# Performance work log

Measured on AMD Instinct MI355X. Metric: run time of the kernel, lower is better.

## Reference

```python
import jax, jax.numpy as jnp
import numpy as np

# graph sizes: G graphs of N_PER nodes each (block-diagonal batched graph)
G, N_PER, F, NHID, E_PER = 128, 512, 128, 128, 4096
N = G * N_PER
E = G * E_PER
L1, L2, L3 = 4, 2, 2            # PANConv filter sizes (conv1 uses init filter_size=4)
K1, K2, K3 = N_PER // 2, N_PER // 4, N_PER // 8  # ratio=0.5 top-k per pooling stage


def setup_inputs() -> dict:
    ks = jax.random.split(jax.random.key(0), 10)
    rng = np.random.default_rng(0)
    off = (np.arange(G) * N_PER)[:, None]
    src = (rng.integers(0, N_PER, size=(G, E_PER)) + off).reshape(-1)
    dst = (rng.integers(0, N_PER, size=(G, E_PER)) + off).reshape(-1)
    edge_index = jnp.asarray(np.stack([src, dst]).astype(np.int32))
    batch = jnp.repeat(jnp.arange(G, dtype=jnp.int32), N_PER)
    def w(k, shp, fan):
        return jax.random.normal(k, shp, jnp.float32) / np.float32(np.sqrt(fan))
    z = lambda *s: jnp.zeros(s, jnp.float32)
    return dict(
        x=jax.random.normal(ks[0], (N, F), jnp.float32),
        edge_index=edge_index, batch=batch,
        lump_W=w(ks[1], (F, NHID), F), lump_b=z(NHID),
        conv1_W=w(ks[2], (NHID, NHID), NHID), conv1_b=z(NHID),
        conv2_W=w(ks[3], (NHID, NHID), NHID), conv2_b=z(NHID),
        conv3_W=w(ks[4], (NHID, NHID), NHID), conv3_b=z(NHID),
        pool1_p=w(ks[5], (NHID,), NHID), pool1_beta=jnp.full((2,), 0.5, jnp.float32),
        pool2_p=w(ks[6], (NHID,), NHID), pool2_beta=jnp.full((2,), 0.5, jnp.float32),
        pool3_p=w(ks[7], (NHID,), NHID), pool3_beta=jnp.full((2,), 0.5, jnp.float32),
        lin1_W=w(ks[8], (NHID, NHID // 2), NHID), lin1_b=z(NHID // 2),
        lin2_W=w(ks[9], (NHID // 2, 1), NHID // 2), lin2_b=z(1),
    )


def _pan_prop(h, src, dst, ew, L):
    # (sum_{l=0..L} A^l) @ h, A weighted by edge weights ew, via iterated gather/scatter
    acc, y = h, h
    n = h.shape[0]
    for _ in range(L):
        y = jax.ops.segment_sum(y[src] * ew[:, None], dst, num_segments=n)
        acc = acc + y
    return acc


def _pan_conv(x, src, dst, ew, W, b, L):
    # PANConv: M = Z^{-1/2} (sum_{l<=L} A^l) Z^{-1/2};  out = M x W + b
    d = _pan_prop(jnp.ones((x.shape[0], 1), x.dtype), src, dst, ew, L)[:, 0]
    dinv = jax.lax.rsqrt(jnp.maximum(d, 1e-12))
    h = dinv[:, None] * _pan_prop(dinv[:, None] * x, src, dst, ew, L)
    return h @ W + b


def _pan_pool(x, src, dst, ew, p, beta, n_per, k):
    # PANPooling: score = beta0*(x.p)/||p|| + beta1*node_strength; per-graph top-k
    n = x.shape[0]
    deg = jax.ops.segment_sum(ew, dst, num_segments=n)
    score = beta[0] * (x @ p) / jnp.linalg.norm(p) + beta[1] * deg
    _, idx = jax.lax.top_k(score.reshape(G, n_per), k)          # [G, k] local indices
    perm = (idx + (jnp.arange(G) * n_per)[:, None]).reshape(-1)  # [G*k] global
    x_new = x[perm] * jnp.tanh(score[perm])[:, None]
    inv = jnp.zeros((n,), jnp.int32).at[perm].set(jnp.arange(G * k, dtype=jnp.int32))
    mask = jnp.zeros((n,), x.dtype).at[perm].set(1.0)
    # keep edge arrays fixed-size: dropped edges get weight 0 (same math as filtering)
    return x_new, inv[src], inv[dst], ew * mask[src] * mask[dst], perm


def reference(x, edge_index, batch, lump_W, lump_b, conv1_W, conv1_b, conv2_W, conv2_b,
              conv3_W, conv3_b, pool1_p, pool1_beta, pool2_p, pool2_beta, pool3_p,
              pool3_beta, lin1_W, lin1_b, lin2_W, lin2_b):
    src, dst = edge_index[0], edge_index[1]
    ew = jnp.ones((src.shape[0],), x.dtype)
    h = x @ lump_W + lump_b                                   # PANLump lift
    h = _pan_conv(h, src, dst, ew, conv1_W, conv1_b, L1)
    h, src, dst, ew, perm1 = _pan_pool(h, src, dst, ew, pool1_p, pool1_beta, N_PER, K1)
    h = _pan_conv(h, src, dst, ew, conv2_W, conv2_b, L2)
    h, src, dst, ew, perm2 = _pan_pool(h, src, dst, ew, pool2_p, pool2_beta, K1, K2)
    h = _pan_conv(h, src, dst, ew, conv3_W, conv3_b, L3)
    h, src, dst, ew, perm3 = _pan_pool(h, src, dst, ew, pool3_p, pool3_beta, K2, K3)
    seg = jnp.repeat(jnp.arange(G, dtype=jnp.int32), K3)
    mean = jax.ops.segment_sum(h, seg, num_segments=G) / jnp.float32(K3)  # scatter_mean
    out = jax.nn.relu(mean @ lin1_W + lin1_b) @ lin2_W + lin2_b           # [G, 1]
    return out
```

## Files before the change

### kernel.cpp

```cpp
#include <hip/hip_runtime.h>
#include <math.h>

#define G_     128
#define E_     524288
#define EPG    4096
#define DEGMAX 48

typedef __attribute__((ext_vector_type(8))) short bf16x8;
typedef __attribute__((ext_vector_type(4))) float f32x4;
typedef __attribute__((ext_vector_type(4))) unsigned short u16x4;

__device__ inline void split_bf16(float x, short& hi, short& lo){
    unsigned u = __float_as_uint(x);
    hi = (short)(u >> 16);
    float hf = __uint_as_float(u & 0xffff0000u);
    unsigned r = __float_as_uint(x - hf);
    lo = (short)(r >> 16);
}

template<int WAVES>
__device__ void gemm_body(char* smem, int bid, const float* __restrict__ X,
        const float* __restrict__ W, const float* __restrict__ bias, float* __restrict__ Y,
        const float* __restrict__ p, const float* __restrict__ beta,
        const int* __restrict__ cntv, float* __restrict__ score){
    short* wsh = (short*)smem;
    short* wsl = (short*)(smem + 34816);
    float* bsh = (float*)(smem + 69632);
    float* qs  = (float*)(smem + 70144);
    float* rednorm = (float*)(smem + 70656);
    const int NT = WAVES*64;
    int t = threadIdx.x;
    for (int e = t; e < 16384; e += NT){
        int k = e >> 7, n = e & 127;
        short hi, lo; split_bf16(W[e], hi, lo);
        wsh[n*136 + k] = hi; wsl[n*136 + k] = lo;
    }
    if (t < 128) bsh[t] = bias[t];
    if (score && t < 64){ float a = p[t], b = p[t+64]; rednorm[t] = a*a + b*b; }
    __syncthreads();
    float b1 = 0.f;
    if (score){
        if (t == 0){ float s = 0.f; for (int i = 0; i < 64; i++) s += rednorm[i]; rednorm[0] = sqrtf(s); }
        __syncthreads();
        if (t < 128) qs[t] = beta[0] * p[t] / rednorm[0];
        b1 = beta[1];
        __syncthreads();
    }
    int wave = t >> 6, lane = t & 63;
    int ln = lane & 15, q = lane >> 4;
    size_t rb = (size_t)bid * (WAVES*16);
    const float* xrow = &X[(rb + wave*16 + ln)*128 + q*8];
    f32x4 acc[8];
    #pragma unroll
    for (int i = 0; i < 8; i++) acc[i] = (f32x4){0.f,0.f,0.f,0.f};
    #pragma unroll
    for (int kc = 0; kc < 4; kc++){
        float4 xa = *(const float4*)(xrow + kc*32);
        float4 xb = *(const float4*)(xrow + kc*32 + 4);
        bf16x8 ah, al; short hi, lo;
        split_bf16(xa.x, hi, lo); ah[0]=hi; al[0]=lo;
        split_bf16(xa.y, hi, lo); ah[1]=hi; al[1]=lo;
        split_bf16(xa.z, hi, lo); ah[2]=hi; al[2]=lo;
        split_bf16(xa.w, hi, lo); ah[3]=hi; al[3]=lo;
        split_bf16(xb.x, hi, lo); ah[4]=hi; al[4]=lo;
        split_bf16(xb.y, hi, lo); ah[5]=hi; al[5]=lo;
        split_bf16(xb.z, hi, lo); ah[6]=hi; al[6]=lo;
        split_bf16(xb.w, hi, lo); ah[7]=hi; al[7]=lo;
        #pragma unroll
        for (int nt = 0; nt < 8; nt++){
            int wo = (nt*16 + ln)*136 + kc*32 + q*8;
            bf16x8 bh = *(const bf16x8*)&wsh[wo];
            bf16x8 bl = *(const bf16x8*)&wsl[wo];
            acc[nt] = __builtin_amdgcn_mfma_f32_16x16x32_bf16(ah, bh, acc[nt], 0, 0, 0);
            acc[nt] = __builtin_amdgcn_mfma_f32_16x16x32_bf16(ah, bl, acc[nt], 0, 0, 0);
            acc[nt] = __builtin_amdgcn_mfma_f32_16x16x32_bf16(al, bh, acc[nt], 0, 0, 0);
        }
    }
    #pragma unroll
    for (int nt = 0; nt < 8; nt++){
        int c = nt*16 + ln;
        float bb = bsh[c];
        #pragma unroll
        for (int r = 0; r < 4; r++){
            Y[(rb + wave*16 + q*4 + r)*128 + c] = acc[nt][r] + bb;
        }
    }
    if (score){
        #pragma unroll
        for (int r = 0; r < 4; r++){
            float sp = 0.f;
            #pragma unroll
            for (int nt = 0; nt < 8; nt++){
                int c = nt*16 + ln;
                sp += (acc[nt][r] + bsh[c]) * qs[c];
            }
            sp += __shfl_xor(sp, 1);
            sp += __shfl_xor(sp, 2);
            sp += __shfl_xor(sp, 4);
            sp += __shfl_xor(sp, 8);
            if (ln == 0){
                int row = (int)rb + wave*16 + q*4 + r;
                score[row] = sp + b1 * (float)cntv[row];
            }
        }
    }
}

template<int WAVES>
__global__ __launch_bounds__(WAVES*64) void k_gemm_mfma(const float* __restrict__ X,
        const float* __restrict__ W, const float* __restrict__ bias, float* __restrict__ Y,
        const float* __restrict__ p, const float* __restrict__ beta,
        const int* __restrict__ cntv, float* __restrict__ score){
    __shared__ __align__(16) char smem[70912];
    gemm_body<WAVES>(smem, blockIdx.x, X, W, bias, Y, p, beta, cntv, score);
}

__global__ __launch_bounds__(512) void k_prep1(const int* __restrict__ ei,
        int* __restrict__ cnt, unsigned short* __restrict__ csrcp,
        int* __restrict__ permg, float* __restrict__ dinvg){
    __shared__ int   lcnt[512];
    __shared__ __align__(16) unsigned short csrS[512*DEGMAX + 8];
    __shared__ float y[1024];
    __shared__ int   bins[64];
    __shared__ int   permS[512];
    int g = blockIdx.x, t = threadIdx.x, gbase = g*512;
    lcnt[t] = 0;
    if (t < 64) bins[t] = 0;
    unsigned* c32 = (unsigned*)csrS;
    for (int i = t; i < 512*DEGMAX/2 + 4; i += 512) c32[i] = 0;
    __syncthreads();
    for (int i = t; i < EPG; i += 512){
        int e = g*EPG + i;
        int sv = ei[e] & 511;
        int d  = ei[E_ + e] & 511;
        int slot = atomicAdd(&lcnt[d], 1);
        if (slot < DEGMAX) csrS[d*DEGMAX + slot] = (unsigned short)sv;
    }
    __syncthreads();
    {
        unsigned* dst = (unsigned*)(csrcp + (size_t)gbase*DEGMAX);
        for (int i = t; i < 512*DEGMAX/2; i += 512) dst[i] = c32[i];
    }
    int rawc = lcnt[t];
    cnt[gbase + t] = rawc;
    int dc = min(rawc, DEGMAX);
    atomicAdd(&bins[dc], 1);
    __syncthreads();
    if (t < 64){
        int v0 = bins[t], s = v0;
        #pragma unroll
        for (int off = 1; off < 64; off <<= 1){
            int n = __shfl_up(s, off);
            if (t >= off) s += n;
        }
        bins[t] = s - v0;
    }
    __syncthreads();
    {
        int slot = atomicAdd(&bins[dc], 1);
        int pk = t | (dc << 16);
        permS[slot] = pk;
        permg[gbase + slot] = pk;
    }
    __syncthreads();
    int pk = permS[t];
    int pv = pk & 0xffff, pd = pk >> 16;
    y[pv] = 1.f;
    __syncthreads();
    float dacc = 1.f;
    int cur = 0;
    for (int l = 0; l < 4; l++){
        const float* la = &y[cur*512];
        float s = 0.f;
        int nq = (pd + 3) >> 2;
        const u16x4* cp = (const u16x4*)(csrS + pv*DEGMAX);
        u16x4 oc = cp[0];
        #pragma unroll 1
        for (int jq = 0; jq < nq; jq++){
            u16x4 ocn = cp[jq + 1];
            s += (la[(int)oc[0]] + la[(int)oc[1]]) + (la[(int)oc[2]] + la[(int)oc[3]]);
            oc = ocn;
        }
        if (nq) s -= (float)(nq*4 - pd) * la[0];
        y[(1^cur)*512 + pv] = s;
        dacc += s;
        __syncthreads();
        cur ^= 1;
    }
    dinvg[gbase + pv] = rsqrtf(fmaxf(dacc, 1e-12f));
}

template<int NPER, int L, int IT, bool SEL>
__global__ __launch_bounds__(1024)
void k_prop(const int* __restrict__ permg, const float* __restrict__ dinvg,
        const unsigned short* __restrict__ csrcp,
        const float* __restrict__ X, const int* __restrict__ selg,
        const float* __restrict__ thg, float* __restrict__ OUT){
    __shared__ __align__(16) float y[NPER*32];
    __shared__ float dinvs[NPER];
    int g = blockIdx.x, fq = blockIdx.y, gbase = g*NPER;
    int t = threadIdx.x;
    int f4 = (t & 7)*4;
    int fo = fq*32 + f4;
    if (t < NPER) dinvs[t] = dinvg[gbase + t];
    int pkr[IT];
    {
        int wv = t >> 6, gi = (t >> 3) & 7;
        #pragma unroll
        for (int it = 0; it < IT; it++){
            int ch = (it & 1) ? (15 - wv) : wv;
            pkr[it] = permg[gbase + (16*it + ch)*8 + gi];
        }
    }
    __syncthreads();
    float4 acc[IT];
    #pragma unroll
    for (int it = 0; it < IT; it++){
        int v = pkr[it] & 0xffff;
        float d = dinvs[v];
        size_t row;
        if (SEL){
            row = (size_t)selg[gbase + v];
            d *= thg[gbase + v];
        } else {
            row = (size_t)(gbase + v);
        }
        float4 w = *(const float4*)&X[row*128 + fo];
        w.x*=d; w.y*=d; w.z*=d; w.w*=d;
        acc[it] = w;
        *(float4*)&y[v*32 + f4] = w;
    }
    __syncthreads();
    for (int l = 0; l < L; l++){
        float4 s[IT];
        #pragma unroll
        for (int it = 0; it < IT; it++){
            int pk = pkr[it];
            int c = pk >> 16;
            int nq = (c + 3) >> 2;
            const u16x4* cp = (const u16x4*)(csrcp + (size_t)(gbase + (pk & 0xffff))*DEGMAX);
            float4 ss = make_float4(0.f,0.f,0.f,0.f);
            u16x4 oc = cp[0];
            #pragma unroll 1
            for (int jq = 0; jq < nq; jq++){
                u16x4 ocn = cp[jq + 1];
                float4 w0 = *(const float4*)&y[((int)oc[0])*32 + f4];
                float4 w1 = *(const float4*)&y[((int)oc[1])*32 + f4];
                float4 w2 = *(const float4*)&y[((int)oc[2])*32 + f4];
                float4 w3 = *(const float4*)&y[((int)oc[3])*32 + f4];
                ss.x += (w0.x + w1.x) + (w2.x + w3.x);
                ss.y += (w0.y + w1.y) + (w2.y + w3.y);
                ss.z += (w0.z + w1.z) + (w2.z + w3.z);
                ss.w += (w0.w + w1.w) + (w2.w + w3.w);
                oc = ocn;
            }
            if (nq){
                float fp = (float)(nq*4 - c);
                float4 z = *(const float4*)&y[f4];
                ss.x -= fp*z.x; ss.y -= fp*z.y; ss.z -= fp*z.z; ss.w -= fp*z.w;
            }
            s[it] = ss;
        }
        __syncthreads();
        #pragma unroll
        for (int it = 0; it < IT; it++){
            int v = pkr[it] & 0xffff;
            *(float4*)&y[v*32 + f4] = s[it];
            acc[it].x+=s[it].x; acc[it].y+=s[it].y; acc[it].z+=s[it].z; acc[it].w+=s[it].w;
        }
        __syncthreads();
    }
    #pragma unroll
    for (int it = 0; it < IT; it++){
        int v = pkr[it] & 0xffff;
        float d = dinvs[v];
        float4 w = acc[it];
        w.x*=d; w.y*=d; w.z*=d; w.w*=d;
        *(float4*)&OUT[(size_t)(gbase + v)*128 + fo] = w;
    }
}

template<int NPER, bool BUILD>
__global__ __launch_bounds__(512) void k_pooltop(const float* __restrict__ score_in,
        const int* __restrict__ esrc_in, const int* __restrict__ edst_in,
        int* __restrict__ esrc_out, int* __restrict__ edst_out,
        int* __restrict__ cnt_next, unsigned short* __restrict__ csrcp,
        int* __restrict__ permg, float* __restrict__ dinvg,
        int* __restrict__ selg, float* __restrict__ thg){
    __shared__ __align__(16) float sc[NPER];
    __shared__ int  nid[NPER];
    __shared__ int  lcnt[NPER/2];
    __shared__ int  bins[64];
    __shared__ int  permS[NPER/2];
    const int K = NPER/2;
    int g = blockIdx.x, t = threadIdx.x, gbase = g*NPER;
    if (t < K) lcnt[t] = 0;
    if (t < 64) bins[t] = 0;
    if (t < NPER) sc[t] = score_in[gbase + t];
    __syncthreads();
    if (t < NPER){
        float s = sc[t];
        int rank = 0;
        const float4* sc4 = (const float4*)sc;
        #pragma unroll 8
        for (int j4 = 0; j4 < NPER/4; j4++){
            float4 v = sc4[j4];
            int j = j4*4;
            rank += (v.x > s) || (v.x == s && (j+0) < t);
            rank += (v.y > s) || (v.y == s && (j+1) < t);
            rank += (v.z > s) || (v.z == s && (j+2) < t);
            rank += (v.w > s) || (v.w == s && (j+3) < t);
        }
        if (rank < K){
            nid[t] = g*K + rank;
            selg[g*K + rank] = gbase + t;
            thg[g*K + rank]  = tanhf(s);
        } else nid[t] = -1;
    }
    __syncthreads();
    if (BUILD){
        for (int i = t; i < EPG; i += 512){
            int e = g*EPG + i;
            int d = edst_in[e];
            if (d < 0) continue;
            int s_ = esrc_in[e];
            int ns = nid[s_ - gbase], nd = nid[d - gbase];
            if ((ns | nd) < 0){ edst_out[e] = -1; }
            else {
                esrc_out[e] = ns; edst_out[e] = nd;
                int slot = atomicAdd(&lcnt[nd & (K-1)], 1);
                if (slot < DEGMAX) csrcp[(size_t)nd*DEGMAX + slot] = (unsigned short)(ns & (K-1));
            }
        }
        __syncthreads();
        float* yd = sc;
        int rawc = 0, dc = 0;
        if (t < K){
            rawc = lcnt[t];
            cnt_next[g*K + t] = rawc;
            dc = min(rawc, DEGMAX);
            int e4 = (dc + 3) & ~3;
            for (int s2 = dc; s2 < e4; s2++) csrcp[(size_t)(g*K + t)*DEGMAX + s2] = 0;
            atomicAdd(&bins[dc], 1);
        }
        __syncthreads();
        if (t < 64){
            int v0 = bins[t], s = v0;
            #pragma unroll
            for (int off = 1; off < 64; off <<= 1){
                int n = __shfl_up(s, off);
                if (t >= off) s += n;
            }
            bins[t] = s - v0;
        }
        __syncthreads();
        if (t < K){
            int slot = atomicAdd(&bins[dc], 1);
            permS[slot] = t | (dc << 16);
            permg[g*K + slot] = permS[slot];
        }
        __syncthreads();
        int pv = 0, pd = 0;
        if (t < K){
            int pk = permS[t];
            pv = pk & 0xffff; pd = pk >> 16;
            yd[pv] = 1.f;
        }
        __syncthreads();
        float dacc = 1.f;
        int cur = 0;
        for (int l = 0; l < 2; l++){
            if (t < K){
                const float* la = &yd[cur*K];
                float s = 0.f;
                int nq = (pd + 3) >> 2;
                const u16x4* cp = (const u16x4*)(csrcp + (size_t)(g*K + pv)*DEGMAX);
                u16x4 oc = cp[0];
                #pragma unroll 1
                for (int jq = 0; jq < nq; jq++){
                    u16x4 ocn = cp[jq + 1];
                    s += (la[(int)oc[0]] + la[(int)oc[1]]) + (la[(int)oc[2]] + la[(int)oc[3]]);
                    oc = ocn;
                }
                if (nq) s -= (float)(nq*4 - pd) * la[0];
                yd[(1^cur)*K + pv] = s;
                dacc += s;
            }
            __syncthreads();
            cur ^= 1;
        }
        if (t < K) dinvg[g*K + pv] = rsqrtf(fmaxf(dacc, 1e-12f));
    }
}

__global__ __launch_bounds__(512) void k_stage3(const float* __restrict__ X,
        const float* __restrict__ W, const float* __restrict__ bias,
        const float* __restrict__ p, const float* __restrict__ beta,
        const int* __restrict__ cntv,
        const float* __restrict__ W1, const float* __restrict__ b1,
        const float* __restrict__ W2, const float* __restrict__ b2,
        float* __restrict__ out){
    __shared__ __align__(16) char smem[70912];
    __shared__ float scs[128];
    __shared__ float thS[64];
    __shared__ int   selS[64];
    __shared__ float mr[128];
    short* wsh = (short*)smem;
    short* wsl = (short*)(smem + 34816);
    float* bsh = (float*)(smem + 69632);
    float* qs  = (float*)(smem + 70144);
    float* rednorm = (float*)(smem + 70656);
    int g = blockIdx.x, t = threadIdx.x;
    for (int e = t; e < 16384; e += 512){
        int k = e >> 7, n = e & 127;
        short hi, lo; split_bf16(W[e], hi, lo);
        wsh[n*136 + k] = hi; wsl[n*136 + k] = lo;
    }
    if (t < 128) bsh[t] = bias[t];
    if (t < 64){ float a = p[t], b = p[t+64]; rednorm[t] = a*a + b*b; }
    __syncthreads();
    if (t == 0){ float s = 0.f; for (int i = 0; i < 64; i++) s += rednorm[i]; rednorm[0] = sqrtf(s); }
    __syncthreads();
    if (t < 128) qs[t] = beta[0] * p[t] / rednorm[0];
    float b1v = beta[1];
    __syncthreads();
    int wave = t >> 6, lane = t & 63;
    int ln = lane & 15, q = lane >> 4;
    const float* xrow = &X[((size_t)g*128 + wave*16 + ln)*128 + q*8];
    f32x4 acc[8];
    #pragma unroll
    for (int i = 0; i < 8; i++) acc[i] = (f32x4){0.f,0.f,0.f,0.f};
    #pragma unroll
    for (int kc = 0; kc < 4; kc++){
        float4 xa = *(const float4*)(xrow + kc*32);
        float4 xb = *(const float4*)(xrow + kc*32 + 4);
        bf16x8 ah, al; short hi, lo;
        split_bf16(xa.x, hi, lo); ah[0]=hi; al[0]=lo;
        split_bf16(xa.y, hi, lo); ah[1]=hi; al[1]=lo;
        split_bf16(xa.z, hi, lo); ah[2]=hi; al[2]=lo;
        split_bf16(xa.w, hi, lo); ah[3]=hi; al[3]=lo;
        split_bf16(xb.x, hi, lo); ah[4]=hi; al[4]=lo;
        split_bf16(xb.y, hi, lo); ah[5]=hi; al[5]=lo;
        split_bf16(xb.z, hi, lo); ah[6]=hi; al[6]=lo;
        split_bf16(xb.w, hi, lo); ah[7]=hi; al[7]=lo;
        #pragma unroll
        for (int nt = 0; nt < 8; nt++){
            int wo = (nt*16 + ln)*136 + kc*32 + q*8;
            bf16x8 bh = *(const bf16x8*)&wsh[wo];
            bf16x8 bl = *(const bf16x8*)&wsl[wo];
            acc[nt] = __builtin_amdgcn_mfma_f32_16x16x32_bf16(ah, bh, acc[nt], 0, 0, 0);
            acc[nt] = __builtin_amdgcn_mfma_f32_16x16x32_bf16(ah, bl, acc[nt], 0, 0, 0);
            acc[nt] = __builtin_amdgcn_mfma_f32_16x16x32_bf16(al, bh, acc[nt], 0, 0, 0);
        }
    }
    #pragma unroll
    for (int r = 0; r < 4; r++){
        float sp = 0.f;
        #pragma unroll
        for (int nt = 0; nt < 8; nt++){
            int c = nt*16 + ln;
            sp += (acc[nt][r] + bsh[c]) * qs[c];
        }
        sp += __shfl_xor(sp, 1);
        sp += __shfl_xor(sp, 2);
        sp += __shfl_xor(sp, 4);
        sp += __shfl_xor(sp, 8);
        if (ln == 0){
            int rl = wave*16 + q*4 + r;
            scs[rl] = sp + b1v * (float)cntv[g*128 + rl];
        }
    }
    __syncthreads();
    float* Yl = (float*)smem;
    #pragma unroll
    for (int nt = 0; nt < 8; nt++){
        int c = nt*16 + ln;
        float bb = bsh[c];
        #pragma unroll
        for (int r = 0; r < 4; r++){
            Yl[(wave*16 + q*4 + r)*132 + c] = acc[nt][r] + bb;
        }
    }
    __syncthreads();
    if (t < 128){
        float s = scs[t];
        int rank = 0;
        const float4* sc4 = (const float4*)scs;
        #pragma unroll 8
        for (int j4 = 0; j4 < 32; j4++){
            float4 v = sc4[j4];
            int j = j4*4;
            rank += (v.x > s) || (v.x == s && (j+0) < t);
            rank += (v.y > s) || (v.y == s && (j+1) < t);
            rank += (v.z > s) || (v.z == s && (j+2) < t);
            rank += (v.w > s) || (v.w == s && (j+3) < t);
        }
        if (rank < 64){ selS[rank] = t; thS[rank] = tanhf(s); }
    }
    __syncthreads();
    if (t < 128){
        float s = 0.f;
        #pragma unroll 8
        for (int r = 0; r < 64; r++) s += Yl[selS[r]*132 + t] * thS[r];
        mr[t] = s * (1.f/64.f);
    }
    __syncthreads();
    if (t < 64){
        float a = b1[t];
        #pragma unroll 8
        for (int k = 0; k < 128; k++) a += mr[k]*W1[k*64 + t];
        a = fmaxf(a, 0.f);
        float r = a * W2[t];
        #pragma unroll
        for (int off = 32; off > 0; off >>= 1) r += __shfl_down(r, off);
        if (t == 0) out[g] = r + b2[0];
    }
}

extern "C" void kernel_launch(void* const* d_in, const int* in_sizes, int n_in,
                              void* d_out, int out_size, void* d_ws, size_t ws_size,
                              hipStream_t stream){
    (void)in_sizes; (void)n_in; (void)out_size; (void)ws_size;
    const float* x     = (const float*)d_in[0];
    const int*   ei    = (const int*)d_in[1];
    const float* lumpW = (const float*)d_in[3];
    const float* lumpb = (const float*)d_in[4];
    const float* convW[3]    = {(const float*)d_in[5], (const float*)d_in[7], (const float*)d_in[9]};
    const float* convB[3]    = {(const float*)d_in[6], (const float*)d_in[8], (const float*)d_in[10]};
    const float* poolP[3]    = {(const float*)d_in[11], (const float*)d_in[13], (const float*)d_in[15]};
    const float* poolBeta[3] = {(const float*)d_in[12], (const float*)d_in[14], (const float*)d_in[16]};
    const float* lin1W = (const float*)d_in[17];
    const float* lin1b = (const float*)d_in[18];
    const float* lin2W = (const float*)d_in[19];
    const float* lin2b = (const float*)d_in[20];
    float* out = (float*)d_out;

    char* w8 = (char*)d_ws;
    size_t off = 0;
    auto alloc = [&](size_t bytes)->char*{
        char* p = w8 + off; off += (bytes + 255) & ~(size_t)255; return p;
    };
    float* A     = (float*)alloc((size_t)65536*128*4);
    float* Bb    = (float*)alloc((size_t)65536*128*4);
    int*   srcA  = (int*)alloc((size_t)E_*4);
    int*   dstA  = (int*)alloc((size_t)E_*4);
    unsigned short* csr1 = (unsigned short*)alloc((size_t)65536*DEGMAX*2);
    unsigned short* csr2 = (unsigned short*)alloc((size_t)32768*DEGMAX*2);
    unsigned short* csr3 = (unsigned short*)alloc((size_t)16384*DEGMAX*2);
    int*   cntA  = (int*)alloc((size_t)(65536+32768+16384)*4);
    int*   cnt1 = cntA, *cnt2 = cntA + 65536, *cnt3 = cntA + 98304;
    int*   perm1 = (int*)alloc((size_t)65536*4);
    int*   perm2 = (int*)alloc((size_t)32768*4);
    int*   perm3 = (int*)alloc((size_t)16384*4);
    float* dinv1 = (float*)alloc((size_t)65536*4);
    float* dinv2 = (float*)alloc((size_t)32768*4);
    float* dinv3 = (float*)alloc((size_t)16384*4);
    float* score1 = (float*)alloc((size_t)65536*4);
    float* score2 = (float*)alloc((size_t)32768*4);
    int*   sel2  = (int*)alloc((size_t)32768*4);
    int*   sel3  = (int*)alloc((size_t)16384*4);
    float* th2   = (float*)alloc((size_t)32768*4);
    float* th3   = (float*)alloc((size_t)16384*4);

    k_prep1<<<G_, 512, 0, stream>>>(ei, cnt1, csr1, perm1, dinv1);
    k_gemm_mfma<8><<<512, 512, 0, stream>>>(x, lumpW, lumpb, A,
            nullptr, nullptr, nullptr, nullptr);

    k_prop<512,4,4,false><<<dim3(G_,4), 1024, 0, stream>>>(perm1, dinv1, csr1, A,
            nullptr, nullptr, Bb);
    k_gemm_mfma<8><<<512, 512, 0, stream>>>(Bb, convW[0], convB[0], A,
            poolP[0], poolBeta[0], cnt1, score1);
    k_pooltop<512,true><<<G_, 512, 0, stream>>>(score1, ei, ei + E_, srcA, dstA,
            cnt2, csr2, perm2, dinv2, sel2, th2);

    k_prop<256,2,2,true><<<dim3(G_,4), 1024, 0, stream>>>(perm2, dinv2, csr2, A,
            sel2, th2, Bb);
    k_gemm_mfma<8><<<256, 512, 0, stream>>>(Bb, convW[1], convB[1], A,
            poolP[1], poolBeta[1], cnt2, score2);
    k_pooltop<256,true><<<G_, 512, 0, stream>>>(score2, srcA, dstA, srcA, dstA,
            cnt3, csr3, perm3, dinv3, sel3, th3);

    k_prop<128,2,1,true><<<dim3(G_,4), 1024, 0, stream>>>(perm3, dinv3, csr3, A,
            sel3, th3, Bb);
    k_stage3<<<G_, 512, 0, stream>>>(Bb, convW[2], convB[2],
            poolP[2], poolBeta[2], cnt3, lin1W, lin1b, lin2W, lin2b, out);
}
```

Before: 276.9 us.

## Swizzle propagation LDS rows and build pooled CSR in shared memory

The propagation kernel's LDS feature buffer gets an XOR swizzle on the float4 column index, keyed by node id, to reduce bank conflicts on gathered neighbour rows. The pool kernel now builds the next-level CSR neighbour list in a zero-initialised shared array and copies it to global memory with coalesced 32-bit stores. This replaces scattered 16-bit global writes and the per-row padding loop. Its own degree propagation also reads the CSR from LDS instead of global memory. The cost is extra LDS per block (about 24KB at the largest size), which may reduce occupancy.

```diff
diff --git a/kernel.cpp b/kernel.cpp
--- a/kernel.cpp
+++ b/kernel.cpp
@@ -17,6 +17,8 @@
     unsigned r = __float_as_uint(x - hf);
     lo = (short)(r >> 16);
 }
+
+__device__ inline int ysw(int v, int f4){ return v*32 + (f4 ^ ((v & 7) << 2)); }
 
 template<int WAVES>
 __device__ void gemm_body(char* smem, int bid, const float* __restrict__ X,
@@ -228,7 +230,7 @@
         float4 w = *(const float4*)&X[row*128 + fo];
         w.x*=d; w.y*=d; w.z*=d; w.w*=d;
         acc[it] = w;
-        *(float4*)&y[v*32 + f4] = w;
+        *(float4*)&y[ysw(v, f4)] = w;
     }
     __syncthreads();
     for (int l = 0; l < L; l++){
@@ -244,10 +246,10 @@
             #pragma unroll 1
             for (int jq = 0; jq < nq; jq++){
                 u16x4 ocn = cp[jq + 1];
-                float4 w0 = *(const float4*)&y[((int)oc[0])*32 + f4];
-                float4 w1 = *(const float4*)&y[((int)oc[1])*32 + f4];
-                float4 w2 = *(const float4*)&y[((int)oc[2])*32 + f4];
-                float4 w3 = *(const float4*)&y[((int)oc[3])*32 + f4];
+                float4 w0 = *(const float4*)&y[ysw((int)oc[0], f4)];
+                float4 w1 = *(const float4*)&y[ysw((int)oc[1], f4)];
+                float4 w2 = *(const float4*)&y[ysw((int)oc[2], f4)];
+                float4 w3 = *(const float4*)&y[ysw((int)oc[3], f4)];
                 ss.x += (w0.x + w1.x) + (w2.x + w3.x);
                 ss.y += (w0.y + w1.y) + (w2.y + w3.y);
                 ss.z += (w0.z + w1.z) + (w2.z + w3.z);
@@ -265,7 +267,7 @@
         #pragma unroll
         for (int it = 0; it < IT; it++){
             int v = pkr[it] & 0xffff;
-            *(float4*)&y[v*32 + f4] = s[it];
+            *(float4*)&y[ysw(v, f4)] = s[it];
             acc[it].x+=s[it].x; acc[it].y+=s[it].y; acc[it].z+=s[it].z; acc[it].w+=s[it].w;
         }
         __syncthreads();
@@ -287,15 +289,21 @@
         int* __restrict__ cnt_next, unsigned short* __restrict__ csrcp,
         int* __restrict__ permg, float* __restrict__ dinvg,
         int* __restrict__ selg, float* __restrict__ thg){
+    const int K = NPER/2;
+    constexpr int CSRSZ = BUILD ? (NPER/2)*DEGMAX + 8 : 8;
     __shared__ __align__(16) float sc[NPER];
     __shared__ int  nid[NPER];
     __shared__ int  lcnt[NPER/2];
     __shared__ int  bins[64];
     __shared__ int  permS[NPER/2];
-    const int K = NPER/2;
+    __shared__ __align__(16) unsigned short csrS[CSRSZ];
     int g = blockIdx.x, t = threadIdx.x, gbase = g*NPER;
     if (t < K) lcnt[t] = 0;
     if (t < 64) bins[t] = 0;
+    if (BUILD){
+        unsigned* c32 = (unsigned*)csrS;
+        for (int i = t; i < K*DEGMAX/2 + 4; i += 512) c32[i] = 0;
+    }
     if (t < NPER) sc[t] = score_in[gbase + t];
     __syncthreads();
     if (t < NPER){
@@ -328,19 +336,23 @@
             if ((ns | nd) < 0){ edst_out[e] = -1; }
             else {
                 esrc_out[e] = ns; edst_out[e] = nd;
-                int slot = atomicAdd(&lcnt[nd & (K-1)], 1);
-                if (slot < DEGMAX) csrcp[(size_t)nd*DEGMAX + slot] = (unsigned short)(ns & (K-1));
-            }
-        }
-        __syncthreads();
+                int ndl = nd & (K-1);
+                int slot = atomicAdd(&lcnt[ndl], 1);
+                if (slot < DEGMAX) csrS[ndl*DEGMAX + slot] = (unsigned short)(ns & (K-1));
+            }
+        }
+        __syncthreads();
+        {
+            unsigned* c32 = (unsigned*)csrS;
+            unsigned* dst = (unsigned*)(csrcp + (size_t)g*K*DEGMAX);
+            for (int i = t; i < K*DEGMAX/2; i += 512) dst[i] = c32[i];
+        }
         float* yd = sc;
         int rawc = 0, dc = 0;
         if (t < K){
             rawc = lcnt[t];
             cnt_next[g*K + t] = rawc;
             dc = min(rawc, DEGMAX);
-            int e4 = (dc + 3) & ~3;
-            for (int s2 = dc; s2 < e4; s2++) csrcp[(size_t)(g*K + t)*DEGMAX + s2] = 0;
             atomicAdd(&bins[dc], 1);
         }
         __syncthreads();
@@ -374,7 +386,7 @@
                 const float* la = &yd[cur*K];
                 float s = 0.f;
                 int nq = (pd + 3) >> 2;
-                const u16x4* cp = (const u16x4*)(csrcp + (size_t)(g*K + pv)*DEGMAX);
+                const u16x4* cp = (const u16x4*)(csrS + pv*DEGMAX);
                 u16x4 oc = cp[0];
                 #pragma unroll 1
                 for (int jq = 0; jq < nq; jq++){
```

Result: slower. 284.1 us (+2.6%).
